# Kernel optimization log

Hardware: AMD Instinct MI355X
Metric: run time of the kernel (lower is better)

The kernel has to match this reference:

```python
import jax, jax.numpy as jnp
import numpy as np

NUM_HEADS = 64
HEAD_DIM = 10  # forced by nn.Linear(10, 1)


def setup_inputs() -> dict:
    key = jax.random.key(0)
    kq, kk, kv, kw = jax.random.split(key, 4)
    B, T, M = 16, 4096, NUM_HEADS * HEAD_DIM
    return {
        "query": jax.random.normal(kq, (B, T, M), dtype=jnp.float32),
        "key": jax.random.normal(kk, (B, T, M), dtype=jnp.float32),
        "value": jax.random.normal(kv, (B, T, M), dtype=jnp.float32),
        "W": jax.random.normal(kw, (1, HEAD_DIM), dtype=jnp.float32) * 0.3,
        "b": jnp.zeros((1,), dtype=jnp.float32),
    }


def _to_heads(x):
    # torch: stack(split(x, head_dim, dim=2), dim=0) -> [H, B, T, D]
    B, T, M = x.shape
    return x.reshape(B, T, NUM_HEADS, HEAD_DIM).transpose(2, 0, 1, 3)


def reference(query, key, value, W, b):
    D = HEAD_DIM
    q = _to_heads(query)   # [H,B,T,D]
    k = _to_heads(key)     # [H,B,T,D]
    v = _to_heads(value)   # [H,B,T,D]
    # key.transpose(-1,-2).sum(3).unsqueeze(2): sum over T -> [H,B,1,D]
    k_sum = k.sum(axis=2, keepdims=True)
    attn = jax.nn.softmax(jnp.tanh(q * k_sum / np.float32(np.sqrt(D))), axis=-1)
    t = attn * v                          # [H,B,T,D]
    v_q = t.sum(axis=2)                   # [H,B,D]
    v_v = t.sum(axis=3).transpose(1, 0, 2)  # [B,H,T]
    # input_proj: Linear(10,1) on v_q*v_q (v_query == v_key == t summed over T)
    s = jnp.tanh((v_q * v_q) @ W.T + b)   # [H,B,1]
    s = jax.nn.softmax(s, axis=-1)        # softmax over size-1 dim (== ones)
    s = s.transpose(1, 0, 2)              # [B,H,1]
    return v_v * s                        # [B,H,T]
```

## Files before the change

### kernel.cpp

```cpp
#include <hip/hip_runtime.h>

#define BB 16
#define TT 4096
#define HH 64
#define DD 10
#define MM 640

#define TROWS 16
#define PADF  161

__global__ void zero_ws_kernel(float* __restrict__ ws, int n) {
    int i = blockIdx.x * blockDim.x + threadIdx.x;
    if (i < n) ws[i] = 0.0f;
}

__global__ void __launch_bounds__(256)
ksum_kernel(const float* __restrict__ key, float* __restrict__ ksum) {
    int g = blockIdx.x * blockDim.x + threadIdx.x;
    int b = g / 160;
    int c = g % 160;
    int t0 = blockIdx.y * 32;

    const float4* p = reinterpret_cast<const float4*>(key)
                    + (size_t)b * TT * 160 + (size_t)t0 * 160 + c;

    float4 a0 = make_float4(0.f,0.f,0.f,0.f);
    float4 a1 = make_float4(0.f,0.f,0.f,0.f);
    float4 a2 = make_float4(0.f,0.f,0.f,0.f);
    float4 a3 = make_float4(0.f,0.f,0.f,0.f);
    #pragma unroll
    for (int i = 0; i < 32; i += 4) {
        float4 x0 = p[(size_t)(i + 0) * 160];
        float4 x1 = p[(size_t)(i + 1) * 160];
        float4 x2 = p[(size_t)(i + 2) * 160];
        float4 x3 = p[(size_t)(i + 3) * 160];
        a0.x += x0.x; a0.y += x0.y; a0.z += x0.z; a0.w += x0.w;
        a1.x += x1.x; a1.y += x1.y; a1.z += x1.z; a1.w += x1.w;
        a2.x += x2.x; a2.y += x2.y; a2.z += x2.z; a2.w += x2.w;
        a3.x += x3.x; a3.y += x3.y; a3.z += x3.z; a3.w += x3.w;
    }
    float sx = (a0.x + a1.x) + (a2.x + a3.x);
    float sy = (a0.y + a1.y) + (a2.y + a3.y);
    float sz = (a0.z + a1.z) + (a2.z + a3.z);
    float sw = (a0.w + a1.w) + (a2.w + a3.w);

    float* dst = ksum + b * MM + c * 4;
    atomicAdd(dst + 0, sx);
    atomicAdd(dst + 1, sy);
    atomicAdd(dst + 2, sz);
    atomicAdd(dst + 3, sw);
}

__device__ __forceinline__ float tanh_fast(float x) {
    float ax = fabsf(x);
    float e2 = __expf(-2.0f * ax);
    float th = (1.0f - e2) / (1.0f + e2);
    return copysignf(th, x);
}

__global__ void __launch_bounds__(128)
attn_kernel(const float* __restrict__ q,
            const float* __restrict__ v,
            const float* __restrict__ ksum,
            float* __restrict__ out) {
    __shared__ float qs[TROWS * PADF];
    __shared__ float vs[TROWS * PADF];

    const int tid = threadIdx.x;
    const int t0  = blockIdx.x * TROWS;
    const int hg  = blockIdx.y;
    const int b   = blockIdx.z;

    const float4* qg = reinterpret_cast<const float4*>(q)
                     + ((size_t)(b * TT + t0)) * 160 + hg * 40;
    const float4* vg = reinterpret_cast<const float4*>(v)
                     + ((size_t)(b * TT + t0)) * 160 + hg * 40;

    float4 rq[5], rv[5];
    #pragma unroll
    for (int i = 0; i < 5; ++i) {
        int idx = tid + 128 * i;
        int row = idx / 40;
        int c   = idx % 40;
        rq[i] = qg[(size_t)row * 160 + c];
        rv[i] = vg[(size_t)row * 160 + c];
    }
    #pragma unroll
    for (int i = 0; i < 5; ++i) {
        int idx  = tid + 128 * i;
        int row  = idx / 40;
        int c    = idx % 40;
        int base = row * PADF + c * 4;
        qs[base + 0] = rq[i].x; qs[base + 1] = rq[i].y;
        qs[base + 2] = rq[i].z; qs[base + 3] = rq[i].w;
        vs[base + 0] = rv[i].x; vs[base + 1] = rv[i].y;
        vs[base + 2] = rv[i].z; vs[base + 3] = rv[i].w;
    }
    __syncthreads();

    const float R = 0.316227766016838f;
    #pragma unroll
    for (int o = 0; o < 2; ++o) {
        int p    = tid + o * 128;
        int row  = p & (TROWS - 1);
        int head = p >> 4;
        const float* ks = ksum + b * MM + hg * 160 + head * 10;

        int lbase = row * PADF + head * 10;
        float sum = 0.f, dot = 0.f;
        #pragma unroll
        for (int d = 0; d < 10; ++d) {
            float e = __expf(tanh_fast(qs[lbase + d] * ks[d] * R));
            sum += e;
            dot += e * vs[lbase + d];
        }
        out[((size_t)(b * HH + hg * 16 + head)) * TT + t0 + row] = dot / sum;
    }
}

extern "C" void kernel_launch(void* const* d_in, const int* in_sizes, int n_in,
                              void* d_out, int out_size, void* d_ws, size_t ws_size,
                              hipStream_t stream) {
    const float* q = (const float*)d_in[0];
    const float* k = (const float*)d_in[1];
    const float* v = (const float*)d_in[2];
    float* out  = (float*)d_out;
    float* ksum = (float*)d_ws;

    zero_ws_kernel<<<dim3((BB * MM + 255) / 256), dim3(256), 0, stream>>>(ksum, BB * MM);
    ksum_kernel<<<dim3(10, 128), dim3(256), 0, stream>>>(k, ksum);
    attn_kernel<<<dim3(TT / TROWS, 4, BB), dim3(128), 0, stream>>>(q, v, ksum, out);
}
```

Measured before the change: 115.8 us.

## Retile attention kernel to full-row tiles with one thread per head

The attention kernel now loads 4 full contiguous rows of q and v (all 64 heads) per 256-thread block into unpadded shared memory, and each thread handles one (row, head) pair. ksum values are held in registers, pre-scaled by 1/sqrt(D). The divides in tanh and in the final normalisation become hardware reciprocals, and the zeroing kernel is replaced with hipMemsetAsync. The aim is fully contiguous global loads and fewer ksum reads, at the cost of possible LDS bank conflicts from the stride-10 access and slightly reduced reciprocal precision.

```diff
diff --git a/kernel.cpp b/kernel.cpp
--- a/kernel.cpp
+++ b/kernel.cpp
@@ -1,18 +1,13 @@
 #include <hip/hip_runtime.h>
+#include <stdint.h>
 
 #define BB 16
 #define TT 4096
 #define HH 64
-#define DD 10
 #define MM 640
 
-#define TROWS 16
-#define PADF  161
-
-__global__ void zero_ws_kernel(float* __restrict__ ws, int n) {
-    int i = blockIdx.x * blockDim.x + threadIdx.x;
-    if (i < n) ws[i] = 0.0f;
-}
+#define ROWS 4
+#define TILE_F4 (ROWS * 160)
 
 __global__ void __launch_bounds__(256)
 ksum_kernel(const float* __restrict__ key, float* __restrict__ ksum) {
@@ -51,71 +46,61 @@
     atomicAdd(dst + 3, sw);
 }
 
-__device__ __forceinline__ float tanh_fast(float x) {
+__device__ __forceinline__ float tanh_rcp(float x) {
     float ax = fabsf(x);
     float e2 = __expf(-2.0f * ax);
-    float th = (1.0f - e2) / (1.0f + e2);
+    float th = (1.0f - e2) * __builtin_amdgcn_rcpf(1.0f + e2);
     return copysignf(th, x);
 }
 
-__global__ void __launch_bounds__(128)
+__global__ void __launch_bounds__(256)
 attn_kernel(const float* __restrict__ q,
             const float* __restrict__ v,
             const float* __restrict__ ksum,
             float* __restrict__ out) {
-    __shared__ float qs[TROWS * PADF];
-    __shared__ float vs[TROWS * PADF];
+    __shared__ float4 s4[2 * TILE_F4];
 
     const int tid = threadIdx.x;
-    const int t0  = blockIdx.x * TROWS;
-    const int hg  = blockIdx.y;
-    const int b   = blockIdx.z;
+    const int t0  = blockIdx.x * ROWS;
+    const int b   = blockIdx.y;
 
-    const float4* qg = reinterpret_cast<const float4*>(q)
-                     + ((size_t)(b * TT + t0)) * 160 + hg * 40;
-    const float4* vg = reinterpret_cast<const float4*>(v)
-                     + ((size_t)(b * TT + t0)) * 160 + hg * 40;
+    const int row  = tid >> 6;
+    const int head = tid & 63;
 
-    float4 rq[5], rv[5];
+    const float R = 0.316227766016838f;
+    float ksr[10];
+    {
+        const float* ks = ksum + b * MM + head * 10;
+        #pragma unroll
+        for (int d = 0; d < 10; ++d) ksr[d] = ks[d] * R;
+    }
+
+    const float4* qt = (const float4*)q + ((size_t)b * TT + t0) * 160;
+    const float4* vt = (const float4*)v + ((size_t)b * TT + t0) * 160;
+
+    float4 rs[5];
     #pragma unroll
     for (int i = 0; i < 5; ++i) {
-        int idx = tid + 128 * i;
-        int row = idx / 40;
-        int c   = idx % 40;
-        rq[i] = qg[(size_t)row * 160 + c];
-        rv[i] = vg[(size_t)row * 160 + c];
+        int idx = tid + 256 * i;
+        rs[i] = (idx < 640) ? qt[idx] : vt[idx - 640];
     }
     #pragma unroll
-    for (int i = 0; i < 5; ++i) {
-        int idx  = tid + 128 * i;
-        int row  = idx / 40;
-        int c    = idx % 40;
-        int base = row * PADF + c * 4;
-        qs[base + 0] = rq[i].x; qs[base + 1] = rq[i].y;
-        qs[base + 2] = rq[i].z; qs[base + 3] = rq[i].w;
-        vs[base + 0] = rv[i].x; vs[base + 1] = rv[i].y;
-        vs[base + 2] = rv[i].z; vs[base + 3] = rv[i].w;
-    }
+    for (int i = 0; i < 5; ++i)
+        s4[tid + 256 * i] = rs[i];
     __syncthreads();
 
-    const float R = 0.316227766016838f;
+    const float* qf = reinterpret_cast<const float*>(s4);
+    const int base = row * MM + head * 10;
+
+    float sum = 0.f, dot = 0.f;
     #pragma unroll
-    for (int o = 0; o < 2; ++o) {
-        int p    = tid + o * 128;
-        int row  = p & (TROWS - 1);
-        int head = p >> 4;
-        const float* ks = ksum + b * MM + hg * 160 + head * 10;
-
-        int lbase = row * PADF + head * 10;
-        float sum = 0.f, dot = 0.f;
-        #pragma unroll
-        for (int d = 0; d < 10; ++d) {
-            float e = __expf(tanh_fast(qs[lbase + d] * ks[d] * R));
-            sum += e;
-            dot += e * vs[lbase + d];
-        }
-        out[((size_t)(b * HH + hg * 16 + head)) * TT + t0 + row] = dot / sum;
+    for (int d = 0; d < 10; ++d) {
+        float e = __expf(tanh_rcp(qf[base + d] * ksr[d]));
+        sum += e;
+        dot += e * qf[2560 + base + d];
     }
+    out[((size_t)(b * HH + head)) * TT + t0 + row]
+        = dot * __builtin_amdgcn_rcpf(sum);
 }
 
 extern "C" void kernel_launch(void* const* d_in, const int* in_sizes, int n_in,
@@ -127,7 +112,7 @@
     float* out  = (float*)d_out;
     float* ksum = (float*)d_ws;
 
-    zero_ws_kernel<<<dim3((BB * MM + 255) / 256), dim3(256), 0, stream>>>(ksum, BB * MM);
+    hipMemsetAsync(d_ws, 0, (size_t)BB * MM * sizeof(float), stream);
     ksum_kernel<<<dim3(10, 128), dim3(256), 0, stream>>>(k, ksum);
-    attn_kernel<<<dim3(TT / TROWS, 4, BB), dim3(128), 0, stream>>>(q, v, ksum, out);
+    attn_kernel<<<dim3(TT / ROWS, BB), dim3(256), 0, stream>>>(q, v, ksum, out);
 }
```

After: 131.3 us. 1.13x slower.
